# Kernel optimization log

Measured on AMD Instinct MI355X. Metric: run time of the kernel, lower is better.

Reference implementation:

```python
import jax, jax.numpy as jnp
import numpy as np

EPS = 1e-5

def _layernorm(x, w, b):
    mu = jnp.mean(x, axis=-1, keepdims=True)
    var = jnp.mean(jnp.square(x - mu), axis=-1, keepdims=True)
    return (x - mu) * jax.lax.rsqrt(var + EPS) * w + b

def setup_inputs() -> dict:
    key = jax.random.key(0)
    ks = jax.random.split(key, 8)
    B, N, C, D = 32, 1024, 4096, 64
    x = jax.random.normal(ks[0], (B, N, C), dtype=jnp.float32)
    gumbel = jax.random.gumbel(ks[1], (B, N, 2), dtype=jnp.float32)
    ln_w = jnp.ones((C,), jnp.float32)
    ln_b = jnp.zeros((C,), jnp.float32)
    w1 = jax.random.normal(ks[2], (C, D), dtype=jnp.float32) * 0.02
    b1 = jnp.zeros((D,), jnp.float32)
    w2 = jax.random.normal(ks[3], (D, 2), dtype=jnp.float32) * 0.02
    b2 = jnp.zeros((2,), jnp.float32)
    return {"x": x, "gumbel": gumbel, "ln_w": ln_w, "ln_b": ln_b,
            "w1": w1, "b1": b1, "w2": w2, "b2": b2}

def reference(x, gumbel, ln_w, ln_b, w1, b1, w2, b2):
    B, N, C = x.shape
    xn = _layernorm(x, ln_w, ln_b)
    local_x = xn[:, :, : C // 2]                      # [B, N, C/2]
    # policy is all-ones -> weighted mean over tokens
    global_x = jnp.mean(xn[:, :, C // 2:], axis=1, keepdims=True)  # [B, 1, C/2]
    feat = jnp.concatenate(
        [local_x, jnp.broadcast_to(global_x, local_x.shape)], axis=-1)  # [B, N, C]
    h = jax.nn.gelu(feat @ w1 + b1, approximate=False)  # [B, N, 64]
    logits = h @ w2 + b2                                # [B, N, 2]
    pred_score = jax.nn.log_softmax(logits, axis=-1)
    # gumbel-softmax (tau=1, hard=True) with straight-through estimator
    y_soft = jax.nn.softmax(pred_score + gumbel, axis=-1)
    hard = jax.nn.one_hot(jnp.argmax(y_soft, axis=-1), 2, dtype=y_soft.dtype)
    y = hard - jax.lax.stop_gradient(y_soft) + y_soft
    keep = y[:, :, 0]                                   # [B, N]
    # dense equivalent of masked_select/split: zero out dropped tokens
    return x * keep[:, :, None]
```

## Files before the change

kernel.cpp:

```cpp
#include <hip/hip_runtime.h>
#include <math.h>

#define B_   32
#define N_   1024
#define C_   4096
#define HC_  2048
#define D_   64
#define NT_  32768
#define KS_  8
#define KC_  (HC_ / KS_)
#define BKC_ 32

__device__ __forceinline__ float4 ld4(const float* p) {
    return *reinterpret_cast<const float4*>(p);
}

__global__ __launch_bounds__(256) void k3_fused(
        const float* __restrict__ x, const float* __restrict__ lnw,
        const float* __restrict__ w1, float* __restrict__ Pp,
        float* __restrict__ spq) {
    __shared__ float As[BKC_ * 256];
    __shared__ float Bsm[BKC_ * D_];

    const int t = threadIdx.x;
    const int mt = blockIdx.x & 127;
    const int ks = blockIdx.x >> 7;
    const int T0 = mt * 256;
    const int kbase = ks * KC_;
    const int rt = t & 63;
    const int dt = t >> 6;
    const int lrow = t >> 3;
    const int lq = t & 7;

    float acc[64];
#pragma unroll
    for (int i = 0; i < 64; ++i) acc[i] = 0.f;
    float sRow[8], qRow[8];
#pragma unroll
    for (int p = 0; p < 8; ++p) { sRow[p] = 0.f; qRow[p] = 0.f; }

    float4 xv[8];
    float4 wv1, wv2;
    float lw1, lw2;
    {
        const int k0 = kbase;
#pragma unroll
        for (int p = 0; p < 8; ++p)
            xv[p] = ld4(x + (size_t)(T0 + lrow + 32 * p) * C_ + k0 + lq * 4);
        const float4* s4 = reinterpret_cast<const float4*>(
            w1 + (size_t)k0 * D_);
        wv1 = s4[t]; wv2 = s4[256 + t];
        lw1 = lnw[k0 + (t >> 4)];
        lw2 = lnw[k0 + 16 + (t >> 4)];
    }

#pragma unroll 1
    for (int kc = 0; kc < KC_ / BKC_; ++kc) {
#pragma unroll
        for (int p = 0; p < 8; ++p) {
            const float4 v = xv[p];
            const int r = lrow + 32 * p;
            const int g = r >> 2, rm = r & 3;
            const int kb = 4 * lq;
            As[(kb + 0) * 256 + (((g ^ ((kb + 0) & 7)) << 2) + rm)] = v.x;
            As[(kb + 1) * 256 + (((g ^ ((kb + 1) & 7)) << 2) + rm)] = v.y;
            As[(kb + 2) * 256 + (((g ^ ((kb + 2) & 7)) << 2) + rm)] = v.z;
            As[(kb + 3) * 256 + (((g ^ ((kb + 3) & 7)) << 2) + rm)] = v.w;
            sRow[p] += (v.x + v.y) + (v.z + v.w);
            qRow[p] = fmaf(v.x, v.x, fmaf(v.y, v.y,
                      fmaf(v.z, v.z, fmaf(v.w, v.w, qRow[p]))));
        }
        {
            float4 v1 = wv1, v2 = wv2;
            v1.x *= lw1; v1.y *= lw1; v1.z *= lw1; v1.w *= lw1;
            v2.x *= lw2; v2.y *= lw2; v2.z *= lw2; v2.w *= lw2;
            float4* b4 = reinterpret_cast<float4*>(Bsm);
            b4[t] = v1;
            b4[256 + t] = v2;
        }
        __syncthreads();
        if (kc + 1 < KC_ / BKC_) {
            const int k1 = kbase + (kc + 1) * BKC_;
#pragma unroll
            for (int p = 0; p < 8; ++p)
                xv[p] = ld4(x + (size_t)(T0 + lrow + 32 * p) * C_
                            + k1 + lq * 4);
            const float4* s4 = reinterpret_cast<const float4*>(
                w1 + (size_t)k1 * D_);
            wv1 = s4[t]; wv2 = s4[256 + t];
            lw1 = lnw[k1 + (t >> 4)];
            lw2 = lnw[k1 + 16 + (t >> 4)];
        }
#pragma unroll 4
        for (int k = 0; k < BKC_; ++k) {
            const float4 a4 = *reinterpret_cast<const float4*>(
                As + k * 256 + ((rt ^ (k & 7)) << 2));
            const float* br = Bsm + k * D_ + dt * 16;
            const float4 b0 = ld4(br), b1 = ld4(br + 4),
                         b2 = ld4(br + 8), b3 = ld4(br + 12);
            const float av[4] = {a4.x, a4.y, a4.z, a4.w};
            const float bv[16] = {b0.x, b0.y, b0.z, b0.w,
                                  b1.x, b1.y, b1.z, b1.w,
                                  b2.x, b2.y, b2.z, b2.w,
                                  b3.x, b3.y, b3.z, b3.w};
#pragma unroll
            for (int ri = 0; ri < 4; ++ri)
#pragma unroll
                for (int cj = 0; cj < 16; ++cj)
                    acc[ri * 16 + cj] =
                        fmaf(av[ri], bv[cj], acc[ri * 16 + cj]);
        }
        __syncthreads();
    }
#pragma unroll
    for (int ri = 0; ri < 4; ++ri) {
        float* dst = Pp + ((size_t)ks * NT_ + T0 + rt * 4 + ri) * D_ + dt * 16;
#pragma unroll
        for (int c = 0; c < 4; ++c)
            *reinterpret_cast<float4*>(dst + c * 4) = make_float4(
                acc[ri * 16 + c * 4], acc[ri * 16 + c * 4 + 1],
                acc[ri * 16 + c * 4 + 2], acc[ri * 16 + c * 4 + 3]);
    }
#pragma unroll
    for (int p = 0; p < 8; ++p) {
        float s = sRow[p], q = qRow[p];
        s += __shfl_xor(s, 1); q += __shfl_xor(q, 1);
        s += __shfl_xor(s, 2); q += __shfl_xor(q, 2);
        s += __shfl_xor(s, 4); q += __shfl_xor(q, 4);
        if (lq == 0) {
            const size_t r = (size_t)(T0 + lrow + 32 * p) * 16;
            spq[r + ks] = s;
            spq[r + 8 + ks] = q;
        }
    }
}

__global__ __launch_bounds__(256) void k1_upper(
        const float* __restrict__ x, const float* __restrict__ lnw,
        const float* __restrict__ lnb, const float* __restrict__ spq,
        float* __restrict__ muv, float* __restrict__ rsv,
        float* __restrict__ part) {
    const int t = threadIdx.x;
    const int lane = t & 63, w = t >> 6;
    const int bid = blockIdx.x;
    const int b = bid >> 5;
    const int g = bid & 31;

    float4 wv[8], bv[8], gacc[8];
#pragma unroll
    for (int m = 0; m < 8; ++m) {
        wv[m] = ld4(lnw + HC_ + (m * 64 + lane) * 4);
        bv[m] = ld4(lnb + HC_ + (m * 64 + lane) * 4);
        gacc[m] = make_float4(0.f, 0.f, 0.f, 0.f);
    }

    for (int i = 0; i < 8; ++i) {
        const int tok = b * N_ + g * 32 + w * 8 + i;
        const float* row = x + (size_t)tok * C_ + HC_;
        float4 v[8];
        float s = 0.f, q = 0.f;
#pragma unroll
        for (int m = 0; m < 8; ++m) {
            v[m] = ld4(row + (m * 64 + lane) * 4);
            s += (v[m].x + v[m].y) + (v[m].z + v[m].w);
            q = fmaf(v[m].x, v[m].x, fmaf(v[m].y, v[m].y,
                fmaf(v[m].z, v[m].z, fmaf(v[m].w, v[m].w, q))));
        }
#pragma unroll
        for (int o = 1; o < 64; o <<= 1) {
            s += __shfl_xor(s, o);
            q += __shfl_xor(q, o);
        }
        const float4 s0 = ld4(spq + (size_t)tok * 16);
        const float4 s1 = ld4(spq + (size_t)tok * 16 + 4);
        const float4 q0 = ld4(spq + (size_t)tok * 16 + 8);
        const float4 q1 = ld4(spq + (size_t)tok * 16 + 12);
        const float S = s + (s0.x + s0.y + s0.z + s0.w)
                          + (s1.x + s1.y + s1.z + s1.w);
        const float Q = q + (q0.x + q0.y + q0.z + q0.w)
                          + (q1.x + q1.y + q1.z + q1.w);
        const float mu = S * (1.f / C_);
        const float rs = rsqrtf(Q * (1.f / C_) - mu * mu + 1e-5f);
        if (lane == 0) {
            muv[tok] = mu;
            rsv[tok] = rs;
        }
#pragma unroll
        for (int m = 0; m < 8; ++m) {
            gacc[m].x += (v[m].x - mu) * rs * wv[m].x + bv[m].x;
            gacc[m].y += (v[m].y - mu) * rs * wv[m].y + bv[m].y;
            gacc[m].z += (v[m].z - mu) * rs * wv[m].z + bv[m].z;
            gacc[m].w += (v[m].w - mu) * rs * wv[m].w + bv[m].w;
        }
    }
    float* pp = part + (size_t)(bid * 4 + w) * HC_;
#pragma unroll
    for (int m = 0; m < 8; ++m)
        *reinterpret_cast<float4*>(pp + (m * 64 + lane) * 4) = gacc[m];
}

__global__ __launch_bounds__(256) void k2a_part(
        const float* __restrict__ part, const float* __restrict__ w1,
        const float* __restrict__ lnw, const float* __restrict__ lnb,
        float* __restrict__ gpart, float* __restrict__ Wpart,
        float* __restrict__ Bpart) {
    __shared__ float Gs[256];
    __shared__ float red[2][4][64];
    const int t = threadIdx.x;
    const int d = t & 63, s = t >> 6;
    const int blk = blockIdx.x;
    if (blk < 256) {
        const int b = blk >> 3, jq = blk & 7;
        const int j = jq * 256 + t;
        float a = 0.f;
        for (int k = 0; k < 128; ++k)
            a += part[(size_t)(b * 128 + k) * HC_ + j];
        Gs[t] = a;
        __syncthreads();
        float acc = 0.f;
        const int j0 = jq * 256 + s * 64;
        for (int jj = 0; jj < 64; ++jj)
            acc = fmaf(Gs[s * 64 + jj],
                       w1[(size_t)(HC_ + j0 + jj) * D_ + d], acc);
        red[0][s][d] = acc;
        __syncthreads();
        if (s == 0)
            gpart[(size_t)blk * 64 + d] =
                red[0][0][d] + red[0][1][d] + red[0][2][d] + red[0][3][d];
    } else {
        const int wq = blk - 256;
        const int c0 = wq * 256 + s * 64;
        float a = 0.f, c2 = 0.f;
        for (int c = c0; c < c0 + 64; ++c) {
            const float wvv = w1[(size_t)c * D_ + d];
            a = fmaf(lnw[c], wvv, a);
            c2 = fmaf(lnb[c], wvv, c2);
        }
        red[0][s][d] = a;
        red[1][s][d] = c2;
        __syncthreads();
        if (s == 0) {
            Wpart[wq * 64 + d] =
                red[0][0][d] + red[0][1][d] + red[0][2][d] + red[0][3][d];
            Bpart[wq * 64 + d] =
                red[1][0][d] + red[1][1][d] + red[1][2][d] + red[1][3][d];
        }
    }
}

__global__ __launch_bounds__(64) void k2b_final(
        const float* __restrict__ gpart, const float* __restrict__ Wpart,
        const float* __restrict__ Bpart, float* __restrict__ gterm,
        float* __restrict__ W1s, float* __restrict__ Bs) {
    const int d = threadIdx.x;
    const int b = blockIdx.x;
    if (b < B_) {
        float a = 0.f;
#pragma unroll
        for (int q = 0; q < 8; ++q)
            a += gpart[(size_t)(b * 8 + q) * 64 + d];
        gterm[b * D_ + d] = a * (1.f / N_);
    } else {
        float a = 0.f, c2 = 0.f;
#pragma unroll
        for (int q = 0; q < 8; ++q) {
            a += Wpart[q * 64 + d];
            c2 += Bpart[q * 64 + d];
        }
        W1s[d] = a;
        Bs[d] = c2;
    }
}

__global__ __launch_bounds__(256) void k45_decide_mask(
        const float* __restrict__ Pp, const float* __restrict__ muv,
        const float* __restrict__ rsv, const float* __restrict__ gterm,
        const float* __restrict__ W1s, const float* __restrict__ Bs,
        const float* __restrict__ b1, const float* __restrict__ w2,
        const float* __restrict__ b2, const float* __restrict__ gum,
        const float* __restrict__ x, float* __restrict__ out) {
    const int t = threadIdx.x;
    const int lane = t & 63, w = t >> 6;
    const int token = blockIdx.x * 4 + w;
    const int b = token >> 10;

    float p = 0.f;
#pragma unroll
    for (int s = 0; s < KS_; ++s)
        p += Pp[((size_t)s * NT_ + token) * D_ + lane];

    const float mu = muv[token], rs = rsv[token];
    float h = rs * (p - mu * W1s[lane]) + Bs[lane] + gterm[b * D_ + lane]
              + b1[lane];
    h = 0.5f * h * (1.f + erff(h * 0.70710678118654752f));
    const float2 w2v = *reinterpret_cast<const float2*>(w2 + lane * 2);
    float l0 = h * w2v.x;
    float l1 = h * w2v.y;
#pragma unroll
    for (int o = 1; o < 64; o <<= 1) {
        l0 += __shfl_xor(l0, o);
        l1 += __shfl_xor(l1, o);
    }
    const float z0 = l0 + b2[0] + gum[token * 2];
    const float z1 = l1 + b2[1] + gum[token * 2 + 1];

    float4* dst = reinterpret_cast<float4*>(out + (size_t)token * C_);
    if (z0 >= z1) {
        const float4* src =
            reinterpret_cast<const float4*>(x + (size_t)token * C_);
#pragma unroll
        for (int c = 0; c < 16; ++c)
            dst[c * 64 + lane] = src[c * 64 + lane];
    } else {
        const float4 z = make_float4(0.f, 0.f, 0.f, 0.f);
#pragma unroll
        for (int c = 0; c < 16; ++c)
            dst[c * 64 + lane] = z;
    }
}

extern "C" void kernel_launch(void* const* d_in, const int* in_sizes, int n_in,
                              void* d_out, int out_size, void* d_ws,
                              size_t ws_size, hipStream_t stream) {
    const float* x   = (const float*)d_in[0];
    const float* gum = (const float*)d_in[1];
    const float* lnw = (const float*)d_in[2];
    const float* lnb = (const float*)d_in[3];
    const float* w1  = (const float*)d_in[4];
    const float* b1  = (const float*)d_in[5];
    const float* w2  = (const float*)d_in[6];
    const float* b2  = (const float*)d_in[7];
    float* out = (float*)d_out;

    float* wsf   = (float*)d_ws;
    float* Pp    = wsf;
    float* muv   = Pp + (size_t)KS_ * NT_ * D_;
    float* rsv   = muv + NT_;
    float* part  = rsv + NT_;
    float* gterm = part + (size_t)4096 * HC_;
    float* W1s   = gterm + B_ * D_;
    float* Bs    = W1s + D_;
    float* spq   = Bs + D_;
    float* gpart = spq + (size_t)NT_ * 16;
    float* Wpart = gpart + 256 * 64;
    float* Bpart = Wpart + 8 * 64;

    k3_fused<<<KS_ * 128, 256, 0, stream>>>(x, lnw, w1, Pp, spq);
    k1_upper<<<1024, 256, 0, stream>>>(x, lnw, lnb, spq, muv, rsv, part);
    k2a_part<<<264, 256, 0, stream>>>(part, w1, lnw, lnb,
                                      gpart, Wpart, Bpart);
    k2b_final<<<33, 64, 0, stream>>>(gpart, Wpart, Bpart, gterm, W1s, Bs);
    k45_decide_mask<<<NT_ / 4, 256, 0, stream>>>(Pp, muv, rsv, gterm, W1s,
                                                 Bs, b1, w2, b2, gum, x, out);
}
```

Baseline: 417.1 us.

## Halve K-split partials and reduce per-wave column sums in shared memory

```diff
diff --git a/kernel.cpp b/kernel.cpp
--- a/kernel.cpp
+++ b/kernel.cpp
@@ -7,7 +7,7 @@
 #define HC_  2048
 #define D_   64
 #define NT_  32768
-#define KS_  8
+#define KS_  4
 #define KC_  (HC_ / KS_)
 #define BKC_ 32
 
@@ -128,9 +128,9 @@
         s += __shfl_xor(s, 2); q += __shfl_xor(q, 2);
         s += __shfl_xor(s, 4); q += __shfl_xor(q, 4);
         if (lq == 0) {
-            const size_t r = (size_t)(T0 + lrow + 32 * p) * 16;
+            const size_t r = (size_t)(T0 + lrow + 32 * p) * 8;
             spq[r + ks] = s;
-            spq[r + 8 + ks] = q;
+            spq[r + 4 + ks] = q;
         }
     }
 }
@@ -140,6 +140,7 @@
         const float* __restrict__ lnb, const float* __restrict__ spq,
         float* __restrict__ muv, float* __restrict__ rsv,
         float* __restrict__ part) {
+    __shared__ float sh[4][HC_];
     const int t = threadIdx.x;
     const int lane = t & 63, w = t >> 6;
     const int bid = blockIdx.x;
@@ -171,14 +172,10 @@
             s += __shfl_xor(s, o);
             q += __shfl_xor(q, o);
         }
-        const float4 s0 = ld4(spq + (size_t)tok * 16);
-        const float4 s1 = ld4(spq + (size_t)tok * 16 + 4);
-        const float4 q0 = ld4(spq + (size_t)tok * 16 + 8);
-        const float4 q1 = ld4(spq + (size_t)tok * 16 + 12);
-        const float S = s + (s0.x + s0.y + s0.z + s0.w)
-                          + (s1.x + s1.y + s1.z + s1.w);
-        const float Q = q + (q0.x + q0.y + q0.z + q0.w)
-                          + (q1.x + q1.y + q1.z + q1.w);
+        const float4 s0 = ld4(spq + (size_t)tok * 8);
+        const float4 q0 = ld4(spq + (size_t)tok * 8 + 4);
+        const float S = s + (s0.x + s0.y) + (s0.z + s0.w);
+        const float Q = q + (q0.x + q0.y) + (q0.z + q0.w);
         const float mu = S * (1.f / C_);
         const float rs = rsqrtf(Q * (1.f / C_) - mu * mu + 1e-5f);
         if (lane == 0) {
@@ -193,10 +190,26 @@
             gacc[m].w += (v[m].w - mu) * rs * wv[m].w + bv[m].w;
         }
     }
-    float* pp = part + (size_t)(bid * 4 + w) * HC_;
 #pragma unroll
     for (int m = 0; m < 8; ++m)
-        *reinterpret_cast<float4*>(pp + (m * 64 + lane) * 4) = gacc[m];
+        *reinterpret_cast<float4*>(&sh[w][(m * 64 + lane) * 4]) = gacc[m];
+    __syncthreads();
+    float* pp = part + (size_t)bid * HC_;
+#pragma unroll
+    for (int m = 0; m < 8; ++m) {
+        const int j = (m * 64 + lane) * 4;
+        const float4 a0 = ld4(&sh[0][j]);
+        const float4 a1 = ld4(&sh[1][j]);
+        const float4 a2 = ld4(&sh[2][j]);
+        const float4 a3 = ld4(&sh[3][j]);
+        float4 r;
+        r.x = (a0.x + a1.x) + (a2.x + a3.x);
+        r.y = (a0.y + a1.y) + (a2.y + a3.y);
+        r.z = (a0.z + a1.z) + (a2.z + a3.z);
+        r.w = (a0.w + a1.w) + (a2.w + a3.w);
+        if (w == (m & 3))
+            *reinterpret_cast<float4*>(pp + j) = r;
+    }
 }
 
 __global__ __launch_bounds__(256) void k2a_part(
@@ -213,8 +226,8 @@
         const int b = blk >> 3, jq = blk & 7;
         const int j = jq * 256 + t;
         float a = 0.f;
-        for (int k = 0; k < 128; ++k)
-            a += part[(size_t)(b * 128 + k) * HC_ + j];
+        for (int k = 0; k < 32; ++k)
+            a += part[(size_t)(b * 32 + k) * HC_ + j];
         Gs[t] = a;
         __syncthreads();
         float acc = 0.f;
@@ -284,6 +297,7 @@
     const int token = blockIdx.x * 4 + w;
     const int b = token >> 10;
 
+    const float2 gv = *reinterpret_cast<const float2*>(gum + token * 2);
     float p = 0.f;
 #pragma unroll
     for (int s = 0; s < KS_; ++s)
@@ -301,8 +315,8 @@
         l0 += __shfl_xor(l0, o);
         l1 += __shfl_xor(l1, o);
     }
-    const float z0 = l0 + b2[0] + gum[token * 2];
-    const float z1 = l1 + b2[1] + gum[token * 2 + 1];
+    const float z0 = l0 + b2[0] + gv.x;
+    const float z1 = l1 + b2[1] + gv.y;
 
     float4* dst = reinterpret_cast<float4*>(out + (size_t)token * C_);
     if (z0 >= z1) {
@@ -337,11 +351,11 @@
     float* muv   = Pp + (size_t)KS_ * NT_ * D_;
     float* rsv   = muv + NT_;
     float* part  = rsv + NT_;
-    float* gterm = part + (size_t)4096 * HC_;
+    float* gterm = part + (size_t)1024 * HC_;
     float* W1s   = gterm + B_ * D_;
     float* Bs    = W1s + D_;
     float* spq   = Bs + D_;
-    float* gpart = spq + (size_t)NT_ * 16;
+    float* gpart = spq + (size_t)NT_ * 8;
     float* Wpart = gpart + 256 * 64;
     float* Bpart = Wpart + 8 * 64;
 
```

After: 407.7 us. 1.02x faster.
